# Kernel optimization log

Hardware: AMD Instinct MI355X
Metric: run time of the kernel (lower is better)

## Reference

```python
import jax, jax.numpy as jnp
import numpy as np

H = 768  # HIDDEN_SIZE


def setup_inputs() -> dict:
    key = jax.random.key(0)
    ks = jax.random.split(key, 6)
    B, T = 32, 1024
    W_SCALE = 0.05  # keep gate pre-activations out of deep saturation
    return {
        "input": jax.random.normal(ks[0], (B, T, H), dtype=jnp.float32),
        "hidden_state": jax.random.normal(ks[1], (1, B, H), dtype=jnp.float32),
        "W_ih": jax.random.normal(ks[2], (3 * H, H), dtype=jnp.float32) * W_SCALE,
        "W_hh": jax.random.normal(ks[3], (3 * H, H), dtype=jnp.float32) * W_SCALE,
        "b_ih": jax.random.normal(ks[4], (3 * H,), dtype=jnp.float32) * W_SCALE,
        "b_hh": jax.random.normal(ks[5], (3 * H,), dtype=jnp.float32) * W_SCALE,
    }


def reference(input, hidden_state, W_ih, W_hh, b_ih, b_hh):
    # PyTorch GRU gate order in the stacked weights is (r, z, n).
    # The module fills bias_ih[H:2H] and bias_hh[H:2H] with -inf, so
    # z_t = sigmoid(-inf) = 0 exactly and h_t = n_t. We therefore skip the
    # structurally-dead z rows entirely (same math, fewer FLOPs):
    #   r_t = sigmoid(W_ir x_t + b_ir + W_hr h_{t-1} + b_hr)
    #   h_t = tanh(W_in x_t + b_in + r_t * (W_hn h_{t-1} + b_hn))
    W_ir, W_in = W_ih[:H], W_ih[2 * H:]          # [H, H] each
    W_hr, W_hn = W_hh[:H], W_hh[2 * H:]
    b_ir, b_in = b_ih[:H], b_ih[2 * H:]
    b_hr, b_hn = b_hh[:H], b_hh[2 * H:]

    # Input projections for all timesteps at once: [B, T, H] each.
    gi_r = jnp.einsum("bth,gh->btg", input, W_ir) + b_ir
    gi_n = jnp.einsum("bth,gh->btg", input, W_in) + b_in

    h0 = hidden_state[0]  # [B, H]

    def step(h, gi_t):
        gi_r_t, gi_n_t = gi_t  # [B, H] each
        r = jax.nn.sigmoid(gi_r_t + h @ W_hr.T + b_hr)
        h_new = jnp.tanh(gi_n_t + r * (h @ W_hn.T + b_hn))
        return h_new, h_new

    # scan over time: move T to leading axis.
    xs = (jnp.swapaxes(gi_r, 0, 1), jnp.swapaxes(gi_n, 0, 1))  # [T, B, H]
    _, hs = jax.lax.scan(step, h0, xs)
    return jnp.swapaxes(hs, 0, 1)  # [B, T, H]
```

## Files before the change

### kernel.cpp

```cpp
#include <hip/hip_runtime.h>
#include <hip/hip_bf16.h>

#define Hd 768
#define Bd 32
#define Td 1024
#define Md (Bd*Td)

#define NPAIR 16
#define SPW   16
#define GPW   48
#define THRS  384
#define RINGD 4
#define SENT_U 0x7FC00000u
#define RVALS (2*Hd)

typedef unsigned int u32x4 __attribute__((ext_vector_type(4)));
typedef float f32x2 __attribute__((ext_vector_type(2)));

static __device__ __forceinline__ f32x2 splat2(float v) { f32x2 r; r.x = v; r.y = v; return r; }

__global__ __launch_bounds__(256) void k_init(const float* __restrict__ hid,
                                              unsigned* __restrict__ ring) {
    int i = blockIdx.x * 256 + threadIdx.x;
    const int p   = i / (RINGD * RVALS);
    const int rem = i % (RINGD * RVALS);
    const int r   = rem / RVALS;
    const int q   = rem % RVALS;
    const int bb  = q / Hd;
    const int k   = q % Hd;
    unsigned v = SENT_U;
    if (r == 0) v = ((const unsigned*)hid)[(p * 2 + bb) * Hd + k];
    ring[i] = v;
}

__global__ __launch_bounds__(256, 2) void k_gemm(const float* __restrict__ A,
                                                 const float* __restrict__ Wih,
                                                 const float* __restrict__ bih,
                                                 float* __restrict__ giR,
                                                 float* __restrict__ giN) {
    __shared__ float As[16][68];
    __shared__ float Brs[16][68];
    __shared__ float Bns[16][68];
    const int tid = threadIdx.x;
    const int mb = blockIdx.x & 511;
    const int nb = blockIdx.x >> 9;
    const int lm = tid >> 2;
    const int lk = (tid & 3) << 2;
    const int tx = tid & 15;
    const int ty = tid >> 4;

    const float* pA = A   + (size_t)(mb * 64 + lm) * Hd + lk;
    const float* pR = Wih + (size_t)(nb * 64 + lm) * Hd + lk;
    const float* pN = Wih + (size_t)(2 * Hd + nb * 64 + lm) * Hd + lk;

    float accR[4][4] = {{0.f}};
    float accN[4][4] = {{0.f}};

    for (int kt = 0; kt < Hd; kt += 16) {
        float4 va = *(const float4*)(pA + kt);
        float4 vr = *(const float4*)(pR + kt);
        float4 vn = *(const float4*)(pN + kt);
        __syncthreads();
        As[lk+0][lm]=va.x; As[lk+1][lm]=va.y; As[lk+2][lm]=va.z; As[lk+3][lm]=va.w;
        Brs[lk+0][lm]=vr.x; Brs[lk+1][lm]=vr.y; Brs[lk+2][lm]=vr.z; Brs[lk+3][lm]=vr.w;
        Bns[lk+0][lm]=vn.x; Bns[lk+1][lm]=vn.y; Bns[lk+2][lm]=vn.z; Bns[lk+3][lm]=vn.w;
        __syncthreads();
        #pragma unroll
        for (int k = 0; k < 16; ++k) {
            float4 a4 = *(const float4*)&As[k][ty << 2];
            float4 r4 = *(const float4*)&Brs[k][tx << 2];
            float4 n4 = *(const float4*)&Bns[k][tx << 2];
            float av[4] = {a4.x, a4.y, a4.z, a4.w};
            float rv[4] = {r4.x, r4.y, r4.z, r4.w};
            float nv[4] = {n4.x, n4.y, n4.z, n4.w};
            #pragma unroll
            for (int i = 0; i < 4; ++i)
                #pragma unroll
                for (int j = 0; j < 4; ++j) {
                    accR[i][j] += av[i] * rv[j];
                    accN[i][j] += av[i] * nv[j];
                }
        }
    }

    const int m0 = mb * 64 + (ty << 2);
    const int g0 = nb * 64 + (tx << 2);
    float4 bR = *(const float4*)(bih + g0);
    float4 bN = *(const float4*)(bih + 2 * Hd + g0);
    #pragma unroll
    for (int i = 0; i < 4; ++i) {
        float4 oR = { accR[i][0]+bR.x, accR[i][1]+bR.y, accR[i][2]+bR.z, accR[i][3]+bR.w };
        float4 oN = { accN[i][0]+bN.x, accN[i][1]+bN.y, accN[i][2]+bN.z, accN[i][3]+bN.w };
        *(float4*)(giR + (size_t)(m0 + i) * Hd + g0) = oR;
        *(float4*)(giN + (size_t)(m0 + i) * Hd + g0) = oN;
    }
}

__global__ __launch_bounds__(THRS, 1) void k_scan(const float* __restrict__ Whh,
                                                  const float* __restrict__ bhh,
                                                  const float* __restrict__ giR,
                                                  float* __restrict__ out,
                                                  unsigned* __restrict__ ring) {
    __shared__ float hs[2 * RVALS];
    const int tid = threadIdx.x;
    const int gl  = tid >> 4;
    const int ks  = tid & 15;
    const int p   = blockIdx.x >> 4;
    const int s   = blockIdx.x & 15;
    const int b0  = p * 2;
    unsigned* ringp = ring + (size_t)p * RINGD * RVALS;

    f32x2 wv[2][48];
    #pragma unroll
    for (int sub = 0; sub < 2; ++sub) {
        const int g = s * GPW + sub * 24 + gl;
        #pragma unroll
        for (int j = 0; j < 12; ++j) {
            float4 a = *(const float4*)(Whh + (size_t)g * Hd + (ks << 2) + (j << 6));
            float4 b = *(const float4*)(Whh + (size_t)(2 * Hd + g) * Hd + (ks << 2) + (j << 6));
            wv[sub][j*4+0].x=a.x; wv[sub][j*4+0].y=b.x;
            wv[sub][j*4+1].x=a.y; wv[sub][j*4+1].y=b.y;
            wv[sub][j*4+2].x=a.z; wv[sub][j*4+2].y=b.z;
            wv[sub][j*4+3].x=a.w; wv[sub][j*4+3].y=b.w;
        }
    }
    #pragma unroll
    for (int sub = 0; sub < 2; ++sub)
        #pragma unroll
        for (int j = 0; j < 48; ++j)
            asm volatile("" : "+v"(wv[sub][j]));

    const int osub = ks & 1, obb = ks >> 1;
    const int og   = s * GPW + osub * 24 + gl;
    float obr = 0.f, obn = 0.f, gRv = 0.f, gNv = 0.f;
    if (ks < 4) {
        obr = bhh[og];
        obn = bhh[2 * Hd + og];
        const size_t mi = ((size_t)(b0 + obb) * Td) * Hd + og;
        gRv = giR[mi];
        gNv = out[mi];
    }

    for (int t = 0; t < Td; ++t) {
        const unsigned* myp = ringp + (t & 3) * RVALS + (tid << 2);
        float* hsl = hs + (t & 1) * RVALS;
        u32x4 w;
        asm volatile("global_load_dwordx4 %0, %1, off sc0 sc1\n\ts_waitcnt vmcnt(0)"
                     : "=v"(w) : "v"(myp) : "memory");
        while (w.x == SENT_U || w.y == SENT_U || w.z == SENT_U || w.w == SENT_U) {
            __builtin_amdgcn_s_sleep(1);
            asm volatile("global_load_dwordx4 %0, %1, off sc0 sc1\n\ts_waitcnt vmcnt(0)"
                         : "=v"(w) : "v"(myp) : "memory");
        }
        *(u32x4*)((unsigned*)hsl + (tid << 2)) = w;

        float gR2 = 0.f, gN2 = 0.f;
        if (ks < 4) {
            const unsigned* rp = ringp + ((t + 2) & 3) * RVALS + obb * Hd + og;
            unsigned sv = SENT_U;
            asm volatile("global_store_dword %0, %1, off sc0 sc1"
                         :: "v"(rp), "v"(sv) : "memory");
            if (t + 1 < Td) {
                const size_t mi = ((size_t)(b0 + obb) * Td + (t + 1)) * Hd + og;
                gR2 = giR[mi];
                gN2 = out[mi];
            }
        }

        __syncthreads();

        f32x2 a2[2][2];
        a2[0][0] = splat2(0.f); a2[0][1] = splat2(0.f);
        a2[1][0] = splat2(0.f); a2[1][1] = splat2(0.f);
        #pragma unroll
        for (int bb = 0; bb < 2; ++bb) {
            #pragma unroll
            for (int j = 0; j < 12; ++j) {
                float4 h4 = *(const float4*)&hsl[bb * Hd + (ks << 2) + (j << 6)];
                #pragma unroll
                for (int sub = 0; sub < 2; ++sub) {
                    a2[sub][bb] = __builtin_elementwise_fma(splat2(h4.x), wv[sub][j*4+0], a2[sub][bb]);
                    a2[sub][bb] = __builtin_elementwise_fma(splat2(h4.y), wv[sub][j*4+1], a2[sub][bb]);
                    a2[sub][bb] = __builtin_elementwise_fma(splat2(h4.z), wv[sub][j*4+2], a2[sub][bb]);
                    a2[sub][bb] = __builtin_elementwise_fma(splat2(h4.w), wv[sub][j*4+3], a2[sub][bb]);
                }
            }
        }
        #pragma unroll
        for (int sub = 0; sub < 2; ++sub)
            #pragma unroll
            for (int bb = 0; bb < 2; ++bb)
                #pragma unroll
                for (int off = 8; off >= 1; off >>= 1) {
                    a2[sub][bb].x += __shfl_xor(a2[sub][bb].x, off);
                    a2[sub][bb].y += __shfl_xor(a2[sub][bb].y, off);
                }

        float hnew = 0.f;
        if (ks < 4) {
            f32x2 mine = osub ? (obb ? a2[1][1] : a2[1][0])
                              : (obb ? a2[0][1] : a2[0][0]);
            const float r = 1.f / (1.f + __expf(-(gRv + mine.x + obr)));
            hnew = tanhf(gNv + r * (mine.y + obn));
            gRv = gR2; gNv = gN2;
        }

        asm volatile("s_waitcnt vmcnt(0)" ::: "memory");

        if (ks < 4) {
            const unsigned* dp = ringp + ((t + 1) & 3) * RVALS + obb * Hd + og;
            const unsigned hbits = __float_as_uint(hnew);
            asm volatile("global_store_dword %0, %1, off sc0 sc1"
                         :: "v"(dp), "v"(hbits) : "memory");
            out[((size_t)(b0 + obb) * Td + t) * Hd + og] = hnew;
        }
    }
}

extern "C" void kernel_launch(void* const* d_in, const int* in_sizes, int n_in,
                              void* d_out, int out_size, void* d_ws, size_t ws_size,
                              hipStream_t stream) {
    const float* input  = (const float*)d_in[0];
    const float* hidden = (const float*)d_in[1];
    const float* Wih    = (const float*)d_in[2];
    const float* Whh    = (const float*)d_in[3];
    const float* bih    = (const float*)d_in[4];
    const float* bhh    = (const float*)d_in[5];
    float* out = (float*)d_out;

    float*    giR  = (float*)d_ws;
    unsigned* ring = (unsigned*)(giR + (size_t)Md * Hd);

    k_init<<<(NPAIR * RINGD * RVALS) / 256, 256, 0, stream>>>(hidden, ring);
    k_gemm<<<512 * 12, 256, 0, stream>>>(input, Wih, bih, giR, out);
    k_scan<<<NPAIR * SPW, THRS, 0, stream>>>(Whh, bhh, giR, out, ring);
}
```

Before: 4.477 ms.

## Move recurrent weights to LDS and process four batches per scan group

```diff
diff --git a/kernel.cpp b/kernel.cpp
--- a/kernel.cpp
+++ b/kernel.cpp
@@ -6,13 +6,16 @@
 #define Td 1024
 #define Md (Bd*Td)
 
-#define NPAIR 16
-#define SPW   16
-#define GPW   48
+#define NGRP 8
+#define SPW   32
+#define RPW   24
+#define BPG   4
 #define THRS  384
 #define RINGD 4
 #define SENT_U 0x7FC00000u
-#define RVALS (2*Hd)
+#define RVALS (BPG*Hd)
+#define WSTRIDE 770
+#define SMEM_BYTES (RPW*WSTRIDE*8 + RVALS*4)
 
 typedef unsigned int u32x4 __attribute__((ext_vector_type(4)));
 typedef float f32x2 __attribute__((ext_vector_type(2)));
@@ -22,14 +25,14 @@
 __global__ __launch_bounds__(256) void k_init(const float* __restrict__ hid,
                                               unsigned* __restrict__ ring) {
     int i = blockIdx.x * 256 + threadIdx.x;
-    const int p   = i / (RINGD * RVALS);
+    const int grp = i / (RINGD * RVALS);
     const int rem = i % (RINGD * RVALS);
     const int r   = rem / RVALS;
     const int q   = rem % RVALS;
     const int bb  = q / Hd;
     const int k   = q % Hd;
     unsigned v = SENT_U;
-    if (r == 0) v = ((const unsigned*)hid)[(p * 2 + bb) * Hd + k];
+    if (r == 0) v = ((const unsigned*)hid)[(grp * BPG + bb) * Hd + k];
     ring[i] = v;
 }
 
@@ -96,72 +99,76 @@
     }
 }
 
-__global__ __launch_bounds__(THRS, 1) void k_scan(const float* __restrict__ Whh,
-                                                  const float* __restrict__ bhh,
-                                                  const float* __restrict__ giR,
-                                                  float* __restrict__ out,
-                                                  unsigned* __restrict__ ring) {
-    __shared__ float hs[2 * RVALS];
+__global__ __launch_bounds__(THRS) void k_scan(const float* __restrict__ Whh,
+                                               const float* __restrict__ bhh,
+                                               const float* __restrict__ giR,
+                                               float* __restrict__ out,
+                                               unsigned* __restrict__ ring) {
+    extern __shared__ char smem[];
+    f32x2* wlds = (f32x2*)smem;
+    float* hs   = (float*)(smem + RPW * WSTRIDE * 8);
+
     const int tid = threadIdx.x;
     const int gl  = tid >> 4;
     const int ks  = tid & 15;
-    const int p   = blockIdx.x >> 4;
-    const int s   = blockIdx.x & 15;
-    const int b0  = p * 2;
-    unsigned* ringp = ring + (size_t)p * RINGD * RVALS;
-
-    f32x2 wv[2][48];
+    const int grp = blockIdx.x >> 5;
+    const int s   = blockIdx.x & 31;
+    const int b0  = grp * BPG;
+    const int g   = s * RPW + gl;
+    unsigned* ringp = ring + (size_t)grp * RINGD * RVALS;
+
     #pragma unroll
-    for (int sub = 0; sub < 2; ++sub) {
-        const int g = s * GPW + sub * 24 + gl;
-        #pragma unroll
-        for (int j = 0; j < 12; ++j) {
-            float4 a = *(const float4*)(Whh + (size_t)g * Hd + (ks << 2) + (j << 6));
-            float4 b = *(const float4*)(Whh + (size_t)(2 * Hd + g) * Hd + (ks << 2) + (j << 6));
-            wv[sub][j*4+0].x=a.x; wv[sub][j*4+0].y=b.x;
-            wv[sub][j*4+1].x=a.y; wv[sub][j*4+1].y=b.y;
-            wv[sub][j*4+2].x=a.z; wv[sub][j*4+2].y=b.z;
-            wv[sub][j*4+3].x=a.w; wv[sub][j*4+3].y=b.w;
-        }
-    }
-    #pragma unroll
-    for (int sub = 0; sub < 2; ++sub)
-        #pragma unroll
-        for (int j = 0; j < 48; ++j)
-            asm volatile("" : "+v"(wv[sub][j]));
-
-    const int osub = ks & 1, obb = ks >> 1;
-    const int og   = s * GPW + osub * 24 + gl;
+    for (int j = 0; j < 12; ++j) {
+        const int kb = (ks << 2) + (j << 6);
+        float4 a = *(const float4*)(Whh + (size_t)g * Hd + kb);
+        float4 b = *(const float4*)(Whh + (size_t)(2 * Hd + g) * Hd + kb);
+        f32x2* wp = wlds + gl * WSTRIDE + kb;
+        f32x2 p0; p0.x = a.x; p0.y = b.x;
+        f32x2 p1; p1.x = a.y; p1.y = b.y;
+        f32x2 p2; p2.x = a.z; p2.y = b.z;
+        f32x2 p3; p3.x = a.w; p3.y = b.w;
+        wp[0] = p0; wp[1] = p1; wp[2] = p2; wp[3] = p3;
+    }
+
+    const int obb = ks;
     float obr = 0.f, obn = 0.f, gRv = 0.f, gNv = 0.f;
     if (ks < 4) {
-        obr = bhh[og];
-        obn = bhh[2 * Hd + og];
-        const size_t mi = ((size_t)(b0 + obb) * Td) * Hd + og;
+        obr = bhh[g];
+        obn = bhh[2 * Hd + g];
+        const size_t mi = ((size_t)(b0 + obb) * Td) * Hd + g;
         gRv = giR[mi];
         gNv = out[mi];
     }
+    __syncthreads();
 
     for (int t = 0; t < Td; ++t) {
-        const unsigned* myp = ringp + (t & 3) * RVALS + (tid << 2);
-        float* hsl = hs + (t & 1) * RVALS;
-        u32x4 w;
-        asm volatile("global_load_dwordx4 %0, %1, off sc0 sc1\n\ts_waitcnt vmcnt(0)"
-                     : "=v"(w) : "v"(myp) : "memory");
-        while (w.x == SENT_U || w.y == SENT_U || w.z == SENT_U || w.w == SENT_U) {
+        const unsigned* myp = ringp + (t & 3) * RVALS + (tid << 3);
+        u32x4 w0, w1;
+        asm volatile(
+            "global_load_dwordx4 %0, %2, off sc0 sc1\n\t"
+            "global_load_dwordx4 %1, %3, off sc0 sc1\n\t"
+            "s_waitcnt vmcnt(0)"
+            : "=&v"(w0), "=&v"(w1) : "v"(myp), "v"(myp + 4) : "memory");
+        while (w0.x == SENT_U || w0.y == SENT_U || w0.z == SENT_U || w0.w == SENT_U ||
+               w1.x == SENT_U || w1.y == SENT_U || w1.z == SENT_U || w1.w == SENT_U) {
             __builtin_amdgcn_s_sleep(1);
-            asm volatile("global_load_dwordx4 %0, %1, off sc0 sc1\n\ts_waitcnt vmcnt(0)"
-                         : "=v"(w) : "v"(myp) : "memory");
-        }
-        *(u32x4*)((unsigned*)hsl + (tid << 2)) = w;
+            asm volatile(
+                "global_load_dwordx4 %0, %2, off sc0 sc1\n\t"
+                "global_load_dwordx4 %1, %3, off sc0 sc1\n\t"
+                "s_waitcnt vmcnt(0)"
+                : "=&v"(w0), "=&v"(w1) : "v"(myp), "v"(myp + 4) : "memory");
+        }
+        *(u32x4*)((unsigned*)hs + (tid << 3))     = w0;
+        *(u32x4*)((unsigned*)hs + (tid << 3) + 4) = w1;
 
         float gR2 = 0.f, gN2 = 0.f;
         if (ks < 4) {
-            const unsigned* rp = ringp + ((t + 2) & 3) * RVALS + obb * Hd + og;
+            const unsigned* rp = ringp + ((t + 2) & 3) * RVALS + obb * Hd + g;
             unsigned sv = SENT_U;
             asm volatile("global_store_dword %0, %1, off sc0 sc1"
                          :: "v"(rp), "v"(sv) : "memory");
             if (t + 1 < Td) {
-                const size_t mi = ((size_t)(b0 + obb) * Td + (t + 1)) * Hd + og;
+                const size_t mi = ((size_t)(b0 + obb) * Td + (t + 1)) * Hd + g;
                 gR2 = giR[mi];
                 gN2 = out[mi];
             }
@@ -169,37 +176,44 @@
 
         __syncthreads();
 
-        f32x2 a2[2][2];
-        a2[0][0] = splat2(0.f); a2[0][1] = splat2(0.f);
-        a2[1][0] = splat2(0.f); a2[1][1] = splat2(0.f);
+        f32x2 a0 = splat2(0.f), a1 = splat2(0.f), a2 = splat2(0.f), a3 = splat2(0.f);
         #pragma unroll
-        for (int bb = 0; bb < 2; ++bb) {
-            #pragma unroll
-            for (int j = 0; j < 12; ++j) {
-                float4 h4 = *(const float4*)&hsl[bb * Hd + (ks << 2) + (j << 6)];
-                #pragma unroll
-                for (int sub = 0; sub < 2; ++sub) {
-                    a2[sub][bb] = __builtin_elementwise_fma(splat2(h4.x), wv[sub][j*4+0], a2[sub][bb]);
-                    a2[sub][bb] = __builtin_elementwise_fma(splat2(h4.y), wv[sub][j*4+1], a2[sub][bb]);
-                    a2[sub][bb] = __builtin_elementwise_fma(splat2(h4.z), wv[sub][j*4+2], a2[sub][bb]);
-                    a2[sub][bb] = __builtin_elementwise_fma(splat2(h4.w), wv[sub][j*4+3], a2[sub][bb]);
-                }
-            }
+        for (int j = 0; j < 12; ++j) {
+            const int kb = (ks << 2) + (j << 6);
+            const f32x2* wp = wlds + gl * WSTRIDE + kb;
+            const f32x2 q0 = wp[0], q1 = wp[1], q2 = wp[2], q3 = wp[3];
+            float4 h0 = *(const float4*)&hs[0 * Hd + kb];
+            float4 h1 = *(const float4*)&hs[1 * Hd + kb];
+            float4 h2 = *(const float4*)&hs[2 * Hd + kb];
+            float4 h3 = *(const float4*)&hs[3 * Hd + kb];
+            a0 = __builtin_elementwise_fma(splat2(h0.x), q0, a0);
+            a0 = __builtin_elementwise_fma(splat2(h0.y), q1, a0);
+            a0 = __builtin_elementwise_fma(splat2(h0.z), q2, a0);
+            a0 = __builtin_elementwise_fma(splat2(h0.w), q3, a0);
+            a1 = __builtin_elementwise_fma(splat2(h1.x), q0, a1);
+            a1 = __builtin_elementwise_fma(splat2(h1.y), q1, a1);
+            a1 = __builtin_elementwise_fma(splat2(h1.z), q2, a1);
+            a1 = __builtin_elementwise_fma(splat2(h1.w), q3, a1);
+            a2 = __builtin_elementwise_fma(splat2(h2.x), q0, a2);
+            a2 = __builtin_elementwise_fma(splat2(h2.y), q1, a2);
+            a2 = __builtin_elementwise_fma(splat2(h2.z), q2, a2);
+            a2 = __builtin_elementwise_fma(splat2(h2.w), q3, a2);
+            a3 = __builtin_elementwise_fma(splat2(h3.x), q0, a3);
+            a3 = __builtin_elementwise_fma(splat2(h3.y), q1, a3);
+            a3 = __builtin_elementwise_fma(splat2(h3.z), q2, a3);
+            a3 = __builtin_elementwise_fma(splat2(h3.w), q3, a3);
         }
         #pragma unroll
-        for (int sub = 0; sub < 2; ++sub)
-            #pragma unroll
-            for (int bb = 0; bb < 2; ++bb)
-                #pragma unroll
-                for (int off = 8; off >= 1; off >>= 1) {
-                    a2[sub][bb].x += __shfl_xor(a2[sub][bb].x, off);
-                    a2[sub][bb].y += __shfl_xor(a2[sub][bb].y, off);
-                }
+        for (int off = 8; off >= 1; off >>= 1) {
+            a0.x += __shfl_xor(a0.x, off); a0.y += __shfl_xor(a0.y, off);
+            a1.x += __shfl_xor(a1.x, off); a1.y += __shfl_xor(a1.y, off);
+            a2.x += __shfl_xor(a2.x, off); a2.y += __shfl_xor(a2.y, off);
+            a3.x += __shfl_xor(a3.x, off); a3.y += __shfl_xor(a3.y, off);
+        }
 
         float hnew = 0.f;
         if (ks < 4) {
-            f32x2 mine = osub ? (obb ? a2[1][1] : a2[1][0])
-                              : (obb ? a2[0][1] : a2[0][0]);
+            f32x2 mine = (ks & 2) ? ((ks & 1) ? a3 : a2) : ((ks & 1) ? a1 : a0);
             const float r = 1.f / (1.f + __expf(-(gRv + mine.x + obr)));
             hnew = tanhf(gNv + r * (mine.y + obn));
             gRv = gR2; gNv = gN2;
@@ -208,12 +222,14 @@
         asm volatile("s_waitcnt vmcnt(0)" ::: "memory");
 
         if (ks < 4) {
-            const unsigned* dp = ringp + ((t + 1) & 3) * RVALS + obb * Hd + og;
+            const unsigned* dp = ringp + ((t + 1) & 3) * RVALS + obb * Hd + g;
             const unsigned hbits = __float_as_uint(hnew);
             asm volatile("global_store_dword %0, %1, off sc0 sc1"
                          :: "v"(dp), "v"(hbits) : "memory");
-            out[((size_t)(b0 + obb) * Td + t) * Hd + og] = hnew;
-        }
+            out[((size_t)(b0 + obb) * Td + t) * Hd + g] = hnew;
+        }
+
+        __syncthreads();
     }
 }
 
@@ -231,7 +247,10 @@
     float*    giR  = (float*)d_ws;
     unsigned* ring = (unsigned*)(giR + (size_t)Md * Hd);
 
-    k_init<<<(NPAIR * RINGD * RVALS) / 256, 256, 0, stream>>>(hidden, ring);
+    hipFuncSetAttribute((const void*)k_scan,
+                        hipFuncAttributeMaxDynamicSharedMemorySize, SMEM_BYTES);
+
+    k_init<<<(NGRP * RINGD * RVALS) / 256, 256, 0, stream>>>(hidden, ring);
     k_gemm<<<512 * 12, 256, 0, stream>>>(input, Wih, bih, giR, out);
-    k_scan<<<NPAIR * SPW, THRS, 0, stream>>>(Whh, bhh, giR, out, ring);
-}
+    k_scan<<<NGRP * SPW, THRS, SMEM_BYTES, stream>>>(Whh, bhh, giR, out, ring);
+}
```

Result: slower. 6.606 ms (+47.6%).
